# Kernel tuning notes

Measured on AMD Instinct MI355X. Metric: run time of the kernel, lower is better.

Reference implementation:

```python
import jax, jax.numpy as jnp
import numpy as np


def setup_inputs() -> dict:
    key = jax.random.key(0)
    k1, k2, k3, k4 = jax.random.split(key, 4)
    N, F, E, M = 50000, 128, 1600000, 1024
    return {
        "molec_feature_vectures": jax.random.normal(k1, (N, F), dtype=jnp.float32),
        "W": jax.random.normal(k2, (F, F), dtype=jnp.float32),
        "mo_neighbour_indices": jax.random.randint(k3, (2, E), 0, N, dtype=jnp.int64),
        "mo_mol_id": jax.random.randint(k4, (E,), 0, M, dtype=jnp.int64),
        "n_output": M,
    }


def reference(molec_feature_vectures, W, mo_neighbour_indices, mo_mol_id, n_output):
    # Gather endpoint features for each neighbor pair: [E, F]
    fi = molec_feature_vectures[mo_neighbour_indices[0]]
    fj = molec_feature_vectures[mo_neighbour_indices[1]]
    # Symmetric bilinear form (mode='pes'): s_n = fi_n . (W + W^T) . fj_n
    Ws = W + W.T  # [F, F]
    # Fuse as (fi @ Ws) * fj summed over F to avoid a 3-operand einsum blowup
    scalars = jnp.einsum('ni,ij,nj->n', fi, Ws, fj)  # [E]
    # Segment-sum per molecule
    res = jax.ops.segment_sum(scalars, mo_mol_id, num_segments=n_output)  # [M]
    return res
```

## Files before the change

kernel.cpp:

```cpp
#include <hip/hip_runtime.h>
#include <hip/hip_bf16.h>

#define FDIM 128
#define BROWS 32
#define NBLK 256

typedef __attribute__((ext_vector_type(8))) short short8v;
typedef __attribute__((ext_vector_type(4))) float f32x4;

static __device__ __forceinline__ unsigned short f2bf(float x) {
    unsigned u = __float_as_uint(x);
    unsigned r = 0x7fffu + ((u >> 16) & 1u);
    return (unsigned short)((u + r) >> 16);
}
static __device__ __forceinline__ float bf2f(unsigned short h) {
    return __uint_as_float((unsigned)h << 16);
}

static __device__ __forceinline__ void split2(float v, short& h, short& l) {
    unsigned short hh = f2bf(v);
    h = (short)hh;
    l = (short)f2bf(v - bf2f(hh));
}

__global__ __launch_bounds__(512, 4) void gemm_mfma(
    const float* __restrict__ Fm, const float* __restrict__ W,
    unsigned short* __restrict__ Gbf, int N) {
    __shared__ unsigned short sH[128 * 136];
    __shared__ unsigned short sL[128 * 136];

    for (int idx = threadIdx.x; idx < 128 * 128; idx += 512) {
        int i = idx >> 7, j = idx & 127;
        float w = W[idx] + W[j * 128 + i];
        short h, l;
        split2(w, h, l);
        sH[i * 136 + j] = (unsigned short)h;
        sL[i * 136 + j] = (unsigned short)l;
    }
    __syncthreads();

    const int wid  = threadIdx.x >> 6;
    const int lane = threadIdx.x & 63;
    const int ar   = lane & 15;
    const int kg   = lane >> 4;
    const int row0 = blockIdx.x * 128 + wid * 16;
    const int gr   = row0 + ar;
    const bool rv  = gr < N;
    const float* fp = Fm + (size_t)gr * FDIM;

    f32x4 acc[8];
#pragma unroll
    for (int t = 0; t < 8; ++t) acc[t] = (f32x4){0.f, 0.f, 0.f, 0.f};

#pragma unroll
    for (int ks = 0; ks < 4; ++ks) {
        const int k0 = ks * 32 + kg * 8;
        float4 fa = make_float4(0.f, 0.f, 0.f, 0.f);
        float4 fb = make_float4(0.f, 0.f, 0.f, 0.f);
        if (rv) {
            fa = *(const float4*)(fp + k0);
            fb = *(const float4*)(fp + k0 + 4);
        }
        short8v ah, al;
        {
            short h, l;
            split2(fa.x, h, l); ah[0] = h; al[0] = l;
            split2(fa.y, h, l); ah[1] = h; al[1] = l;
            split2(fa.z, h, l); ah[2] = h; al[2] = l;
            split2(fa.w, h, l); ah[3] = h; al[3] = l;
            split2(fb.x, h, l); ah[4] = h; al[4] = l;
            split2(fb.y, h, l); ah[5] = h; al[5] = l;
            split2(fb.z, h, l); ah[6] = h; al[6] = l;
            split2(fb.w, h, l); ah[7] = h; al[7] = l;
        }
#pragma unroll
        for (int ct = 0; ct < 8; ++ct) {
            const short8v bh = *(const short8v*)(sH + (ct * 16 + ar) * 136 + k0);
            const short8v bl = *(const short8v*)(sL + (ct * 16 + ar) * 136 + k0);
            acc[ct] = __builtin_amdgcn_mfma_f32_16x16x32_bf16(ah, bh, acc[ct], 0, 0, 0);
            acc[ct] = __builtin_amdgcn_mfma_f32_16x16x32_bf16(ah, bl, acc[ct], 0, 0, 0);
            acc[ct] = __builtin_amdgcn_mfma_f32_16x16x32_bf16(al, bh, acc[ct], 0, 0, 0);
        }
    }

#pragma unroll
    for (int r = 0; r < 4; ++r) {
        const int orow = row0 + kg * 4 + r;
        if (orow < N) {
#pragma unroll
            for (int ct = 0; ct < 8; ++ct)
                Gbf[(size_t)orow * FDIM + ct * 16 + ar] = f2bf(acc[ct][r]);
        }
    }
}

__global__ __launch_bounds__(256) void k_hist(const int* __restrict__ idx, int E,
                                              int nb, unsigned* __restrict__ M,
                                              float* __restrict__ out, int Mout) {
    if (blockIdx.x == 0) {
        for (int i = threadIdx.x; i < Mout; i += 256) out[i] = 0.f;
    }
    extern __shared__ unsigned cnt[];
    for (int i = threadIdx.x; i < nb; i += 256) cnt[i] = 0;
    __syncthreads();
    int chunk = (E + NBLK - 1) / NBLK;
    int s = blockIdx.x * chunk;
    int e_end = min(E, s + chunk);
    for (int e = s + threadIdx.x; e < e_end; e += 256) {
        int i1 = idx[E + e];
        atomicAdd(&cnt[i1 >> 5], 1u);
    }
    __syncthreads();
    for (int i = threadIdx.x; i < nb; i += 256)
        M[(size_t)blockIdx.x * nb + i] = cnt[i];
}

__global__ __launch_bounds__(256) void k_mscan2(unsigned* __restrict__ M, int nb,
                                                unsigned* __restrict__ tot) {
    int b = blockIdx.x * 4 + (threadIdx.x >> 6);
    int lane = threadIdx.x & 63;
    if (b >= nb) return;
    unsigned m0 = M[(size_t)(4 * lane + 0) * nb + b];
    unsigned m1 = M[(size_t)(4 * lane + 1) * nb + b];
    unsigned m2 = M[(size_t)(4 * lane + 2) * nb + b];
    unsigned m3 = M[(size_t)(4 * lane + 3) * nb + b];
    unsigned s = m0 + m1 + m2 + m3;
    unsigned incl = s;
#pragma unroll
    for (int d = 1; d < 64; d <<= 1) {
        unsigned u = __shfl_up(incl, d, 64);
        if (lane >= d) incl += u;
    }
    unsigned run = incl - s;
    M[(size_t)(4 * lane + 0) * nb + b] = run; run += m0;
    M[(size_t)(4 * lane + 1) * nb + b] = run; run += m1;
    M[(size_t)(4 * lane + 2) * nb + b] = run; run += m2;
    M[(size_t)(4 * lane + 3) * nb + b] = run;
    if (lane == 63) tot[b] = incl;
}

__global__ __launch_bounds__(256) void k_bscan(const unsigned* __restrict__ tot, int nb,
                                               unsigned* __restrict__ bucketStart) {
    __shared__ unsigned wS[4];
    int t = threadIdx.x;
    unsigned v0, v1, v2, v3, v4, v5, v6, v7;
    int b0 = t * 8;
    v0 = (b0 + 0 < nb) ? tot[b0 + 0] : 0u;
    v1 = (b0 + 1 < nb) ? tot[b0 + 1] : 0u;
    v2 = (b0 + 2 < nb) ? tot[b0 + 2] : 0u;
    v3 = (b0 + 3 < nb) ? tot[b0 + 3] : 0u;
    v4 = (b0 + 4 < nb) ? tot[b0 + 4] : 0u;
    v5 = (b0 + 5 < nb) ? tot[b0 + 5] : 0u;
    v6 = (b0 + 6 < nb) ? tot[b0 + 6] : 0u;
    v7 = (b0 + 7 < nb) ? tot[b0 + 7] : 0u;
    unsigned l0 = 0, l1 = v0, l2 = l1 + v1, l3 = l2 + v2, l4 = l3 + v3,
             l5 = l4 + v4, l6 = l5 + v5, l7 = l6 + v6;
    unsigned s = l7 + v7;
    int lane = t & 63, wid = t >> 6;
    unsigned incl = s;
    for (int d = 1; d < 64; d <<= 1) {
        unsigned u = __shfl_up(incl, d, 64);
        if (lane >= d) incl += u;
    }
    if (lane == 63) wS[wid] = incl;
    __syncthreads();
    unsigned wOff = 0;
    for (int i = 0; i < wid; ++i) wOff += wS[i];
    unsigned base = wOff + incl - s;
    if (b0 + 0 < nb) bucketStart[b0 + 0] = base + l0;
    if (b0 + 1 < nb) bucketStart[b0 + 1] = base + l1;
    if (b0 + 2 < nb) bucketStart[b0 + 2] = base + l2;
    if (b0 + 3 < nb) bucketStart[b0 + 3] = base + l3;
    if (b0 + 4 < nb) bucketStart[b0 + 4] = base + l4;
    if (b0 + 5 < nb) bucketStart[b0 + 5] = base + l5;
    if (b0 + 6 < nb) bucketStart[b0 + 6] = base + l6;
    if (b0 + 7 < nb) bucketStart[b0 + 7] = base + l7;
    if (t == 255) bucketStart[nb] = base + s;
}

__global__ __launch_bounds__(256) void k_scatter(const int* __restrict__ idx,
                                                 const int* __restrict__ mol, int E,
                                                 int nb, const unsigned* __restrict__ M,
                                                 const unsigned* __restrict__ bucketStart,
                                                 unsigned* __restrict__ sortedE) {
    extern __shared__ unsigned cur[];
    for (int i = threadIdx.x; i < nb; i += 256)
        cur[i] = M[(size_t)blockIdx.x * nb + i] + bucketStart[i];
    __syncthreads();
    int chunk = (E + NBLK - 1) / NBLK;
    int s = blockIdx.x * chunk;
    int e_end = min(E, s + chunk);
    for (int e = s + threadIdx.x; e < e_end; e += 256) {
        int i0 = idx[e];
        int i1 = idx[E + e];
        int m  = mol[e];
        int b  = i1 >> 5;
        int loc = i1 & 31;
        unsigned pos = atomicAdd(&cur[b], 1u);
        sortedE[pos] = (unsigned)i0 | ((unsigned)m << 16) | ((unsigned)loc << 26);
    }
}

__global__ __launch_bounds__(512, 8) void edge_kernel(
    const unsigned short* __restrict__ Gbf, const float* __restrict__ Fm,
    const unsigned* __restrict__ sortedE, const unsigned* __restrict__ bucketStart,
    float* __restrict__ out, int N, int Mout) {
    __shared__ __align__(16) unsigned short sFrow[BROWS * FDIM];
    __shared__ float smol[1024];

    const int b = blockIdx.x;
    const int row0 = b * BROWS;
    const int nrow = min(BROWS, N - row0);

    for (int k = threadIdx.x; k < nrow * 16; k += 512) {
        int r = k >> 4, g = k & 15;
        const float4* src = (const float4*)(Fm + (size_t)(row0 + r) * FDIM + g * 8);
        float4 v0 = src[0], v1 = src[1];
        unsigned u0 = (unsigned)f2bf(v0.x) | ((unsigned)f2bf(v0.y) << 16);
        unsigned u1 = (unsigned)f2bf(v0.z) | ((unsigned)f2bf(v0.w) << 16);
        unsigned u2 = (unsigned)f2bf(v1.x) | ((unsigned)f2bf(v1.y) << 16);
        unsigned u3 = (unsigned)f2bf(v1.z) | ((unsigned)f2bf(v1.w) << 16);
        char* dst = (char*)sFrow + r * 256 + ((g * 16) ^ ((r & 7) << 4));
        *(uint4*)dst = make_uint4(u0, u1, u2, u3);
    }
    for (int i = threadIdx.x; i < 1024; i += 512) smol[i] = 0.f;
    __syncthreads();

    const int s = (int)bucketStart[b];
    const int e_end = (int)bucketStart[b + 1];
    const int lane = threadIdx.x & 63;
    const int wid  = threadIdx.x >> 6;
    const int er = lane & 15;
    const int kg = lane >> 4;
    const bool isdiag = ((er >> 2) == kg);

    int base = s + wid * 16;
    unsigned pk = 0u;
    if (base + er < e_end && base < e_end) pk = sortedE[base + er];

    while (base < e_end) {
        const int nbase = base + 128;
        unsigned npk = 0u;
        if (nbase < e_end && nbase + er < e_end) npk = sortedE[nbase + er];

        const int i0  = pk & 0xffff;
        const int loc = pk >> 26;
        const unsigned short* gp = Gbf + (size_t)i0 * FDIM + kg * 8;
        const char* lp = (const char*)sFrow + loc * 256;
        const int swz = (loc & 7) << 4;

        f32x4 acc = (f32x4){0.f, 0.f, 0.f, 0.f};
#pragma unroll
        for (int ks = 0; ks < 4; ++ks) {
            short8v a  = *(const short8v*)(gp + ks * 32);
            short8v bf = *(const short8v*)(lp + ((ks * 64 + kg * 16) ^ swz));
            acc = __builtin_amdgcn_mfma_f32_16x16x32_bf16(a, bf, acc, 0, 0, 0);
        }
        if (isdiag && (base + er < e_end)) {
            atomicAdd(&smol[(pk >> 16) & 0x3ff], acc[er & 3]);
        }
        pk = npk;
        base = nbase;
    }
    __syncthreads();

    for (int i = threadIdx.x; i < Mout; i += 512) {
        float v = smol[i];
        if (v != 0.f) atomicAdd(&out[i], v);
    }
}

extern "C" void kernel_launch(void* const* d_in, const int* in_sizes, int n_in,
                              void* d_out, int out_size, void* d_ws, size_t ws_size,
                              hipStream_t stream) {
    const float* Fm = (const float*)d_in[0];
    const float* W  = (const float*)d_in[1];
    const int* idx  = (const int*)d_in[2];
    const int* mol  = (const int*)d_in[3];
    float* out = (float*)d_out;

    const int N = in_sizes[0] / FDIM;
    const int E = in_sizes[3];

    const int nb = (N + BROWS - 1) / BROWS;

    char* ws = (char*)d_ws;
    size_t o = 0;
    unsigned short* Gbf = (unsigned short*)(ws + o); o += ((size_t)N * FDIM * 2 + 255) & ~(size_t)255;
    unsigned* sortedE = (unsigned*)(ws + o);         o += ((size_t)E * 4 + 255) & ~(size_t)255;
    unsigned* M = (unsigned*)(ws + o);               o += ((size_t)NBLK * nb * 4 + 255) & ~(size_t)255;
    unsigned* tot = (unsigned*)(ws + o);             o += ((size_t)nb * 4 + 255) & ~(size_t)255;
    unsigned* bucketStart = (unsigned*)(ws + o);     o += ((size_t)(nb + 1) * 4 + 255) & ~(size_t)255;

    gemm_mfma<<<(N + 127) / 128, 512, 0, stream>>>(Fm, W, Gbf, N);

    size_t smem = (size_t)nb * 4;
    k_hist<<<NBLK, 256, smem, stream>>>(idx, E, nb, M, out, out_size);
    k_mscan2<<<(nb + 3) / 4, 256, 0, stream>>>(M, nb, tot);
    k_bscan<<<1, 256, 0, stream>>>(tot, nb, bucketStart);
    k_scatter<<<NBLK, 256, smem, stream>>>(idx, mol, E, nb, M, bucketStart, sortedE);

    edge_kernel<<<nb, 512, 0, stream>>>(Gbf, Fm, sortedE, bucketStart, out, N, out_size);
}
```

Before: 210.5 us.

## Replace MFMA edge dot products with fp16 dot2 lane reductions and resize sort blocks

The per-edge dot product now stores G and the local feature rows in fp16 instead of bf16. Each lane computes packed fdot2 partial sums and then reduces across 16 lanes with shuffles, where before a 16x16 MFMA was issued and only its diagonal was kept. Each wave now processes four edges per lane group with four prefetched index words. The histogram and scatter kernels use 128 blocks of 1024 threads instead of 256 blocks of 256, and the scan is adjusted to match. fp16 has a narrower range than bf16, so large G values could overflow, and the LDS swizzle was removed.

```diff
diff --git a/kernel.cpp b/kernel.cpp
--- a/kernel.cpp
+++ b/kernel.cpp
@@ -3,10 +3,11 @@
 
 #define FDIM 128
 #define BROWS 32
-#define NBLK 256
+#define NBLK 128
 
 typedef __attribute__((ext_vector_type(8))) short short8v;
 typedef __attribute__((ext_vector_type(4))) float f32x4;
+typedef __attribute__((ext_vector_type(2))) _Float16 half2v;
 
 static __device__ __forceinline__ unsigned short f2bf(float x) {
     unsigned u = __float_as_uint(x);
@@ -16,18 +17,35 @@
 static __device__ __forceinline__ float bf2f(unsigned short h) {
     return __uint_as_float((unsigned)h << 16);
 }
-
 static __device__ __forceinline__ void split2(float v, short& h, short& l) {
     unsigned short hh = f2bf(v);
     h = (short)hh;
     l = (short)f2bf(v - bf2f(hh));
 }
 
+static __device__ __forceinline__ half2v u2h(unsigned u) {
+    union { unsigned u; half2v h; } c; c.u = u; return c.h;
+}
+static __device__ __forceinline__ unsigned pack2h(float a, float b) {
+    union { unsigned u; half2v h; } c;
+    c.h[0] = (_Float16)a; c.h[1] = (_Float16)b; return c.u;
+}
+static __device__ __forceinline__ unsigned short f2h(float x) {
+    union { unsigned short s; _Float16 h; } c; c.h = (_Float16)x; return c.s;
+}
+static __device__ __forceinline__ float fdot2(half2v a, half2v b, float c) {
+#if defined(__has_builtin) && __has_builtin(__builtin_amdgcn_fdot2)
+    return __builtin_amdgcn_fdot2(a, b, c, false);
+#else
+    return fmaf((float)a[1], (float)b[1], fmaf((float)a[0], (float)b[0], c));
+#endif
+}
+
 __global__ __launch_bounds__(512, 4) void gemm_mfma(
     const float* __restrict__ Fm, const float* __restrict__ W,
-    unsigned short* __restrict__ Gbf, int N) {
-    __shared__ unsigned short sH[128 * 136];
-    __shared__ unsigned short sL[128 * 136];
+    unsigned short* __restrict__ Gh, int N) {
+    __shared__ __align__(16) unsigned short sH[128 * 136];
+    __shared__ __align__(16) unsigned short sL[128 * 136];
 
     for (int idx = threadIdx.x; idx < 128 * 128; idx += 512) {
         int i = idx >> 7, j = idx & 127;
@@ -89,29 +107,29 @@
         if (orow < N) {
 #pragma unroll
             for (int ct = 0; ct < 8; ++ct)
-                Gbf[(size_t)orow * FDIM + ct * 16 + ar] = f2bf(acc[ct][r]);
-        }
-    }
-}
-
-__global__ __launch_bounds__(256) void k_hist(const int* __restrict__ idx, int E,
-                                              int nb, unsigned* __restrict__ M,
-                                              float* __restrict__ out, int Mout) {
+                Gh[(size_t)orow * FDIM + ct * 16 + ar] = f2h(acc[ct][r]);
+        }
+    }
+}
+
+__global__ __launch_bounds__(1024) void k_hist(const int* __restrict__ idx, int E,
+                                               int nb, unsigned* __restrict__ M,
+                                               float* __restrict__ out, int Mout) {
     if (blockIdx.x == 0) {
-        for (int i = threadIdx.x; i < Mout; i += 256) out[i] = 0.f;
+        for (int i = threadIdx.x; i < Mout; i += 1024) out[i] = 0.f;
     }
     extern __shared__ unsigned cnt[];
-    for (int i = threadIdx.x; i < nb; i += 256) cnt[i] = 0;
+    for (int i = threadIdx.x; i < nb; i += 1024) cnt[i] = 0;
     __syncthreads();
     int chunk = (E + NBLK - 1) / NBLK;
     int s = blockIdx.x * chunk;
     int e_end = min(E, s + chunk);
-    for (int e = s + threadIdx.x; e < e_end; e += 256) {
+    for (int e = s + threadIdx.x; e < e_end; e += 1024) {
         int i1 = idx[E + e];
         atomicAdd(&cnt[i1 >> 5], 1u);
     }
     __syncthreads();
-    for (int i = threadIdx.x; i < nb; i += 256)
+    for (int i = threadIdx.x; i < nb; i += 1024)
         M[(size_t)blockIdx.x * nb + i] = cnt[i];
 }
 
@@ -120,11 +138,9 @@
     int b = blockIdx.x * 4 + (threadIdx.x >> 6);
     int lane = threadIdx.x & 63;
     if (b >= nb) return;
-    unsigned m0 = M[(size_t)(4 * lane + 0) * nb + b];
-    unsigned m1 = M[(size_t)(4 * lane + 1) * nb + b];
-    unsigned m2 = M[(size_t)(4 * lane + 2) * nb + b];
-    unsigned m3 = M[(size_t)(4 * lane + 3) * nb + b];
-    unsigned s = m0 + m1 + m2 + m3;
+    unsigned m0 = M[(size_t)(2 * lane + 0) * nb + b];
+    unsigned m1 = M[(size_t)(2 * lane + 1) * nb + b];
+    unsigned s = m0 + m1;
     unsigned incl = s;
 #pragma unroll
     for (int d = 1; d < 64; d <<= 1) {
@@ -132,10 +148,8 @@
         if (lane >= d) incl += u;
     }
     unsigned run = incl - s;
-    M[(size_t)(4 * lane + 0) * nb + b] = run; run += m0;
-    M[(size_t)(4 * lane + 1) * nb + b] = run; run += m1;
-    M[(size_t)(4 * lane + 2) * nb + b] = run; run += m2;
-    M[(size_t)(4 * lane + 3) * nb + b] = run;
+    M[(size_t)(2 * lane + 0) * nb + b] = run; run += m0;
+    M[(size_t)(2 * lane + 1) * nb + b] = run;
     if (lane == 63) tot[b] = incl;
 }
 
@@ -178,19 +192,19 @@
     if (t == 255) bucketStart[nb] = base + s;
 }
 
-__global__ __launch_bounds__(256) void k_scatter(const int* __restrict__ idx,
-                                                 const int* __restrict__ mol, int E,
-                                                 int nb, const unsigned* __restrict__ M,
-                                                 const unsigned* __restrict__ bucketStart,
-                                                 unsigned* __restrict__ sortedE) {
+__global__ __launch_bounds__(1024) void k_scatter(const int* __restrict__ idx,
+                                                  const int* __restrict__ mol, int E,
+                                                  int nb, const unsigned* __restrict__ M,
+                                                  const unsigned* __restrict__ bucketStart,
+                                                  unsigned* __restrict__ sortedE) {
     extern __shared__ unsigned cur[];
-    for (int i = threadIdx.x; i < nb; i += 256)
+    for (int i = threadIdx.x; i < nb; i += 1024)
         cur[i] = M[(size_t)blockIdx.x * nb + i] + bucketStart[i];
     __syncthreads();
     int chunk = (E + NBLK - 1) / NBLK;
     int s = blockIdx.x * chunk;
     int e_end = min(E, s + chunk);
-    for (int e = s + threadIdx.x; e < e_end; e += 256) {
+    for (int e = s + threadIdx.x; e < e_end; e += 1024) {
         int i0 = idx[e];
         int i1 = idx[E + e];
         int m  = mol[e];
@@ -201,8 +215,8 @@
     }
 }
 
-__global__ __launch_bounds__(512, 8) void edge_kernel(
-    const unsigned short* __restrict__ Gbf, const float* __restrict__ Fm,
+__global__ __launch_bounds__(512, 6) void edge_kernel(
+    const unsigned short* __restrict__ Gh, const float* __restrict__ Fm,
     const unsigned* __restrict__ sortedE, const unsigned* __restrict__ bucketStart,
     float* __restrict__ out, int N, int Mout) {
     __shared__ __align__(16) unsigned short sFrow[BROWS * FDIM];
@@ -216,12 +230,12 @@
         int r = k >> 4, g = k & 15;
         const float4* src = (const float4*)(Fm + (size_t)(row0 + r) * FDIM + g * 8);
         float4 v0 = src[0], v1 = src[1];
-        unsigned u0 = (unsigned)f2bf(v0.x) | ((unsigned)f2bf(v0.y) << 16);
-        unsigned u1 = (unsigned)f2bf(v0.z) | ((unsigned)f2bf(v0.w) << 16);
-        unsigned u2 = (unsigned)f2bf(v1.x) | ((unsigned)f2bf(v1.y) << 16);
-        unsigned u3 = (unsigned)f2bf(v1.z) | ((unsigned)f2bf(v1.w) << 16);
-        char* dst = (char*)sFrow + r * 256 + ((g * 16) ^ ((r & 7) << 4));
-        *(uint4*)dst = make_uint4(u0, u1, u2, u3);
+        uint4 u;
+        u.x = pack2h(v0.x, v0.y);
+        u.y = pack2h(v0.z, v0.w);
+        u.z = pack2h(v1.x, v1.y);
+        u.w = pack2h(v1.z, v1.w);
+        *(uint4*)(sFrow + r * FDIM + g * 8) = u;
     }
     for (int i = threadIdx.x; i < 1024; i += 512) smol[i] = 0.f;
     __syncthreads();
@@ -229,39 +243,74 @@
     const int s = (int)bucketStart[b];
     const int e_end = (int)bucketStart[b + 1];
     const int lane = threadIdx.x & 63;
+    const int sub  = lane >> 4;
+    const int t16  = lane & 15;
+    const int off16 = t16 * 8;
     const int wid  = threadIdx.x >> 6;
-    const int er = lane & 15;
-    const int kg = lane >> 4;
-    const bool isdiag = ((er >> 2) == kg);
+
+#define DOT8(p, g, f) \
+    p = fdot2(u2h((g).x), u2h((f).x), p); \
+    p = fdot2(u2h((g).y), u2h((f).y), p); \
+    p = fdot2(u2h((g).z), u2h((f).z), p); \
+    p = fdot2(u2h((g).w), u2h((f).w), p);
 
     int base = s + wid * 16;
-    unsigned pk = 0u;
-    if (base + er < e_end && base < e_end) pk = sortedE[base + er];
+    unsigned pk0 = 0u, pk1 = 0u, pk2 = 0u, pk3 = 0u;
+    if (base + sub < e_end)      pk0 = sortedE[base + sub];
+    if (base + 4 + sub < e_end)  pk1 = sortedE[base + 4 + sub];
+    if (base + 8 + sub < e_end)  pk2 = sortedE[base + 8 + sub];
+    if (base + 12 + sub < e_end) pk3 = sortedE[base + 12 + sub];
 
     while (base < e_end) {
         const int nbase = base + 128;
-        unsigned npk = 0u;
-        if (nbase < e_end && nbase + er < e_end) npk = sortedE[nbase + er];
-
-        const int i0  = pk & 0xffff;
-        const int loc = pk >> 26;
-        const unsigned short* gp = Gbf + (size_t)i0 * FDIM + kg * 8;
-        const char* lp = (const char*)sFrow + loc * 256;
-        const int swz = (loc & 7) << 4;
-
-        f32x4 acc = (f32x4){0.f, 0.f, 0.f, 0.f};
-#pragma unroll
-        for (int ks = 0; ks < 4; ++ks) {
-            short8v a  = *(const short8v*)(gp + ks * 32);
-            short8v bf = *(const short8v*)(lp + ((ks * 64 + kg * 16) ^ swz));
-            acc = __builtin_amdgcn_mfma_f32_16x16x32_bf16(a, bf, acc, 0, 0, 0);
-        }
-        if (isdiag && (base + er < e_end)) {
-            atomicAdd(&smol[(pk >> 16) & 0x3ff], acc[er & 3]);
-        }
-        pk = npk;
+        unsigned npk0 = 0u, npk1 = 0u, npk2 = 0u, npk3 = 0u;
+        if (nbase + sub < e_end)      npk0 = sortedE[nbase + sub];
+        if (nbase + 4 + sub < e_end)  npk1 = sortedE[nbase + 4 + sub];
+        if (nbase + 8 + sub < e_end)  npk2 = sortedE[nbase + 8 + sub];
+        if (nbase + 12 + sub < e_end) npk3 = sortedE[nbase + 12 + sub];
+
+        const uint4 g0 = *(const uint4*)(Gh + (size_t)(pk0 & 0xffffu) * FDIM + off16);
+        const uint4 g1 = *(const uint4*)(Gh + (size_t)(pk1 & 0xffffu) * FDIM + off16);
+        const uint4 g2 = *(const uint4*)(Gh + (size_t)(pk2 & 0xffffu) * FDIM + off16);
+        const uint4 g3 = *(const uint4*)(Gh + (size_t)(pk3 & 0xffffu) * FDIM + off16);
+        const uint4 f0 = *(const uint4*)(sFrow + (pk0 >> 26) * FDIM + off16);
+        const uint4 f1 = *(const uint4*)(sFrow + (pk1 >> 26) * FDIM + off16);
+        const uint4 f2 = *(const uint4*)(sFrow + (pk2 >> 26) * FDIM + off16);
+        const uint4 f3 = *(const uint4*)(sFrow + (pk3 >> 26) * FDIM + off16);
+
+        float p0 = 0.f, p1 = 0.f, p2 = 0.f, p3 = 0.f;
+        DOT8(p0, g0, f0);
+        DOT8(p1, g1, f1);
+        DOT8(p2, g2, f2);
+        DOT8(p3, g3, f3);
+
+        p0 += __shfl_xor(p0, 1, 16);
+        p1 += __shfl_xor(p1, 1, 16);
+        p2 += __shfl_xor(p2, 1, 16);
+        p3 += __shfl_xor(p3, 1, 16);
+        p0 += __shfl_xor(p0, 2, 16);
+        p1 += __shfl_xor(p1, 2, 16);
+        p2 += __shfl_xor(p2, 2, 16);
+        p3 += __shfl_xor(p3, 2, 16);
+        p0 += __shfl_xor(p0, 4, 16);
+        p1 += __shfl_xor(p1, 4, 16);
+        p2 += __shfl_xor(p2, 4, 16);
+        p3 += __shfl_xor(p3, 4, 16);
+        p0 += __shfl_xor(p0, 8, 16);
+        p1 += __shfl_xor(p1, 8, 16);
+        p2 += __shfl_xor(p2, 8, 16);
+        p3 += __shfl_xor(p3, 8, 16);
+
+        if (t16 == 0) {
+            if (base + sub < e_end)      atomicAdd(&smol[(pk0 >> 16) & 0x3ff], p0);
+            if (base + 4 + sub < e_end)  atomicAdd(&smol[(pk1 >> 16) & 0x3ff], p1);
+            if (base + 8 + sub < e_end)  atomicAdd(&smol[(pk2 >> 16) & 0x3ff], p2);
+            if (base + 12 + sub < e_end) atomicAdd(&smol[(pk3 >> 16) & 0x3ff], p3);
+        }
+        pk0 = npk0; pk1 = npk1; pk2 = npk2; pk3 = npk3;
         base = nbase;
     }
+#undef DOT8
     __syncthreads();
 
     for (int i = threadIdx.x; i < Mout; i += 512) {
@@ -286,19 +335,19 @@
 
     char* ws = (char*)d_ws;
     size_t o = 0;
-    unsigned short* Gbf = (unsigned short*)(ws + o); o += ((size_t)N * FDIM * 2 + 255) & ~(size_t)255;
+    unsigned short* Gh = (unsigned short*)(ws + o);  o += ((size_t)N * FDIM * 2 + 255) & ~(size_t)255;
     unsigned* sortedE = (unsigned*)(ws + o);         o += ((size_t)E * 4 + 255) & ~(size_t)255;
     unsigned* M = (unsigned*)(ws + o);               o += ((size_t)NBLK * nb * 4 + 255) & ~(size_t)255;
     unsigned* tot = (unsigned*)(ws + o);             o += ((size_t)nb * 4 + 255) & ~(size_t)255;
     unsigned* bucketStart = (unsigned*)(ws + o);     o += ((size_t)(nb + 1) * 4 + 255) & ~(size_t)255;
 
-    gemm_mfma<<<(N + 127) / 128, 512, 0, stream>>>(Fm, W, Gbf, N);
+    gemm_mfma<<<(N + 127) / 128, 512, 0, stream>>>(Fm, W, Gh, N);
 
     size_t smem = (size_t)nb * 4;
-    k_hist<<<NBLK, 256, smem, stream>>>(idx, E, nb, M, out, out_size);
+    k_hist<<<NBLK, 1024, smem, stream>>>(idx, E, nb, M, out, out_size);
     k_mscan2<<<(nb + 3) / 4, 256, 0, stream>>>(M, nb, tot);
     k_bscan<<<1, 256, 0, stream>>>(tot, nb, bucketStart);
-    k_scatter<<<NBLK, 256, smem, stream>>>(idx, mol, E, nb, M, bucketStart, sortedE);
-
-    edge_kernel<<<nb, 512, 0, stream>>>(Gbf, Fm, sortedE, bucketStart, out, N, out_size);
-}
+    k_scatter<<<NBLK, 1024, smem, stream>>>(idx, mol, E, nb, M, bucketStart, sortedE);
+
+    edge_kernel<<<nb, 512, 0, stream>>>(Gh, Fm, sortedE, bucketStart, out, N, out_size);
+}
```

Measured after the change: 209.9 us. Within noise of the previous version (-0.3%).
